# Optimization experiments

Measured on AMD Instinct MI355X. Metric: run time of the kernel, lower is better.

Reference implementation:

```python
import jax, jax.numpy as jnp
import numpy as np

D = 4096   # feature_dim
L = 24     # num_vision_layers
H = 8      # num_heads
HD = D // H
R = D // 4 # reduced_dim


def _ln(x, g, b, eps=1e-5):
    m = jnp.mean(x, -1, keepdims=True)
    v = jnp.var(x, -1, keepdims=True)
    return (x - m) * jax.lax.rsqrt(v + eps) * g + b


def setup_inputs() -> dict:
    key = jax.random.key(0)
    ks = jax.random.split(key, 16)
    B, T, N = 1, 128, 576
    def W(k, shape, s=0.02):
        return jax.random.normal(k, shape, jnp.float32) * s
    inp = {
        'text': jax.random.normal(ks[0], (B, T, D), jnp.float32),
        'feats': jax.random.normal(ks[1], (L, B, N, D), jnp.float32),
        'W1_w': W(ks[2], (R, 3 * D)), 'W1_b': jnp.zeros((R,), jnp.float32),
        'Wc_w': W(ks[3], (D, R)), 'Wc_b': jnp.zeros((D,), jnp.float32),
        'Wi_w': W(ks[4], (D, R)), 'Wi_b': jnp.zeros((D,), jnp.float32),
        'Wf_w': W(ks[5], (D, R)), 'Wf_b': jnp.zeros((D,), jnp.float32),
        'bc': jnp.zeros((D,), jnp.float32),
        'bi': jnp.zeros((D,), jnp.float32),
        'bf': jnp.zeros((D,), jnp.float32),
        'g1_w': W(ks[6], (D, D)), 'g1_b': jnp.zeros((D,), jnp.float32),
        'g2_w': W(ks[7], (D, D)), 'g2_b': jnp.zeros((D,), jnp.float32),
        'Wq_w': W(ks[8], (D, D)), 'Wq_b': jnp.zeros((D,), jnp.float32),
        'Wk_w': W(ks[9], (D, D)), 'Wk_b': jnp.zeros((D,), jnp.float32),
        'Wo_w': W(ks[10], (D, D)), 'Wo_b': jnp.zeros((D,), jnp.float32),
        'qn_g': jnp.ones((D,), jnp.float32), 'qn_b': jnp.zeros((D,), jnp.float32),
        'kn_g': jnp.ones((D,), jnp.float32), 'kn_b': jnp.zeros((D,), jnp.float32),
        'on_g': jnp.ones((D,), jnp.float32), 'on_b': jnp.zeros((D,), jnp.float32),
    }
    return inp


def reference(text, feats, W1_w, W1_b, Wc_w, Wc_b, Wi_w, Wi_b, Wf_w, Wf_b,
              bc, bi, bf, g1_w, g1_b, g2_w, g2_b, Wq_w, Wq_b, Wk_w, Wk_b,
              Wo_w, Wo_b, qn_g, qn_b, kn_g, kn_b, on_g, on_b):
    B, T, _ = text.shape
    N = feats.shape[2]
    text_global = jnp.mean(text, axis=1)      # [B, D]
    y = jnp.mean(feats, axis=2)               # [L, B, D]

    # DSU recurrence over L layers (shared weights) via scan
    def step(c_prev, y_l):
        cpn = jax.nn.sigmoid(jax.lax.stop_gradient(c_prev))
        comb = jnp.concatenate([cpn, y_l, text_global], axis=-1)  # [B, 3D]
        s = jax.nn.relu(comb @ W1_w.T + W1_b)                     # [B, R]
        c_tilde = jnp.tanh(s @ Wc_w.T + Wc_b + bc)
        ig = jax.nn.sigmoid(s @ Wi_w.T + Wi_b + bi)
        fg = jax.nn.sigmoid(s @ Wf_w.T + Wf_b + bf)
        c = fg * c_prev + ig * c_tilde
        return c, c

    _, ctx = jax.lax.scan(step, jnp.zeros_like(text_global), y)   # [L, B, D]

    # Spatial gate, vectorized over all L layers (context is detached)
    c_sg = jax.lax.stop_gradient(ctx)[:, :, None, :]              # [L, B, 1, D]
    h = jax.nn.gelu((c_sg + feats) @ g1_w.T + g1_b, approximate=False)
    gate = jax.nn.sigmoid(h @ g2_w.T + g2_b)
    refreshed = feats * gate                                      # [L, B, N, D]

    # Q / K / V
    Q = _ln(text @ Wq_w.T + Wq_b, qn_g, qn_b)
    Q = Q.reshape(B, T, H, HD).transpose(0, 2, 1, 3)              # [B, H, T, HD]
    K = _ln(refreshed @ Wk_w.T + Wk_b, kn_g, kn_b)                # [L, B, N, D]
    K_all = K.reshape(L, B, N, H, HD).transpose(1, 3, 0, 2, 4).reshape(B, H, L * N, HD)
    V_all = refreshed.reshape(L, B, N, H, HD).transpose(1, 3, 0, 2, 4).reshape(B, H, L * N, HD)

    scale = (HD ** 0.5) * (L ** 0.5)
    scores = jnp.einsum('bhtd,bhsd->bhts', Q, K_all) / scale
    attn = jax.nn.softmax(scores, axis=-1)
    att = jnp.einsum('bhts,bhsd->bhtd', attn, V_all)
    att = att.transpose(0, 2, 1, 3).reshape(B, T, D)
    out = _ln(att @ Wo_w.T + Wo_b, on_g, on_b)
    return out
```

## Files before the change

kernel.cpp:

```cpp
#include <hip/hip_runtime.h>

#define USH unsigned short

__device__ __forceinline__ float bf2f(USH u) {
    return __uint_as_float(((unsigned int)u) << 16);
}
__device__ __forceinline__ float bfbits2f(unsigned int b) {
    return __uint_as_float(b << 16);
}
__device__ __forceinline__ USH f2bf(float f) {
    unsigned int x = __float_as_uint(f);
    x += 0x7fffu + ((x >> 16) & 1u);
    return (USH)(x >> 16);
}
__device__ __forceinline__ unsigned int pack2bf(float a, float b) {
    return (unsigned int)f2bf(a) | ((unsigned int)f2bf(b) << 16);
}
__device__ __forceinline__ float sigmoidf_(float x) { return 1.0f / (1.0f + expf(-x)); }

typedef __bf16 bf16x8 __attribute__((ext_vector_type(8)));
typedef float floatx4 __attribute__((ext_vector_type(4)));

#define GLOAD_LDS16(g, l) __builtin_amdgcn_global_load_lds( \
    (const __attribute__((address_space(1))) void*)(g),     \
    (__attribute__((address_space(3))) void*)(l), 16, 0, 0)

enum { EPI_SCORES = 0, EPI_GELU = 1, EPI_GATE = 2, EPI_PLAIN = 3 };

template <int EPI, bool WF32>
__global__ __launch_bounds__(256)
void gemm_bt(const USH* __restrict__ A, int lda, long long sAz, long long sAz2, int zdiv,
             const void* __restrict__ Wv, int ldw, long long sWz, long long sWz2,
             void* __restrict__ Cout, int ldc, long long sCz,
             const float* __restrict__ bias, const float* __restrict__ fmul,
             float alpha, int Kd)
{
    __shared__ USH As[2][128 * 32];
    __shared__ USH Ws[2][128 * 32];
    const int z = blockIdx.z;
    const int z1 = z / zdiv;
    const int z2 = z % zdiv;
    A += (size_t)z1 * (size_t)sAz + (size_t)z2 * (size_t)sAz2;
    const USH* Wb = (const USH*)Wv + (size_t)z1 * (size_t)sWz + (size_t)z2 * (size_t)sWz2;
    const float* Wf = (const float*)Wv;
    const int m0 = blockIdx.y * 128;
    const int n0 = blockIdx.x * 128;
    const int tid = threadIdx.x;
    const int lane = tid & 63;
    const int wid = tid >> 6;
    const int wm = (wid >> 1) * 64;
    const int wn = (wid & 1) * 64;
    const int q = lane >> 4;
    const int r = lane & 15;

    floatx4 acc[4][4] = {};

    const int c0 = wid * 2;
    const int grow = c0 * 16 + (lane >> 2);
    const int gcol = (lane & 3) * 8;
    const USH* apA0 = A + (size_t)(m0 + grow) * lda + gcol;
    const USH* apA1 = apA0 + (size_t)16 * lda;
    USH* lA0 = &As[0][c0 * 512];
    USH* lA1 = &As[0][(c0 + 1) * 512];
    const USH* apW0 = Wb + (size_t)(n0 + grow) * ldw + gcol;
    const USH* apW1 = apW0 + (size_t)16 * ldw;
    USH* lW0 = &Ws[0][c0 * 512];
    USH* lW1 = &Ws[0][(c0 + 1) * 512];

    const int frow = tid >> 1;
    const int fcol = (tid & 1) * 16;
    const float* wpf = Wf + (size_t)(n0 + frow) * ldw + fcol;
    USH* wsw = &Ws[0][frow * 32 + fcol];

    auto stage = [&](int k0, int b) {
        GLOAD_LDS16(apA0 + k0, lA0 + b * 4096);
        GLOAD_LDS16(apA1 + k0, lA1 + b * 4096);
        if constexpr (WF32) {
            float4 f0 = *reinterpret_cast<const float4*>(wpf + k0);
            float4 f1 = *reinterpret_cast<const float4*>(wpf + k0 + 4);
            float4 f2 = *reinterpret_cast<const float4*>(wpf + k0 + 8);
            float4 f3 = *reinterpret_cast<const float4*>(wpf + k0 + 12);
            uint4 w0, w1;
            w0.x = pack2bf(f0.x, f0.y); w0.y = pack2bf(f0.z, f0.w);
            w0.z = pack2bf(f1.x, f1.y); w0.w = pack2bf(f1.z, f1.w);
            w1.x = pack2bf(f2.x, f2.y); w1.y = pack2bf(f2.z, f2.w);
            w1.z = pack2bf(f3.x, f3.y); w1.w = pack2bf(f3.z, f3.w);
            *reinterpret_cast<uint4*>(wsw + b * 4096) = w0;
            *reinterpret_cast<uint4*>(wsw + b * 4096 + 8) = w1;
        } else {
            GLOAD_LDS16(apW0 + k0, lW0 + b * 4096);
            GLOAD_LDS16(apW1 + k0, lW1 + b * 4096);
        }
    };

    auto compute = [&](const USH* Asb, const USH* Wsb) {
        bf16x8 af[4], wf4[4];
#pragma unroll
        for (int i = 0; i < 4; i++)
            af[i] = *reinterpret_cast<const bf16x8*>(&Asb[(wm + i * 16 + r) * 32 + q * 8]);
#pragma unroll
        for (int j = 0; j < 4; j++)
            wf4[j] = *reinterpret_cast<const bf16x8*>(&Wsb[(wn + j * 16 + r) * 32 + q * 8]);
#pragma unroll
        for (int i = 0; i < 4; i++)
#pragma unroll
            for (int j = 0; j < 4; j++)
                acc[i][j] = __builtin_amdgcn_mfma_f32_16x16x32_bf16(af[i], wf4[j], acc[i][j], 0, 0, 0);
    };

    stage(0, 0);
    asm volatile("s_waitcnt vmcnt(0) lgkmcnt(0)" ::: "memory");
    __builtin_amdgcn_s_barrier();

    for (int k0 = 0; k0 < Kd; k0 += 64) {
        stage(k0 + 32, 1);
        compute(&As[0][0], &Ws[0][0]);
        asm volatile("s_waitcnt vmcnt(0) lgkmcnt(0)" ::: "memory");
        __builtin_amdgcn_s_barrier();
        if (k0 + 64 < Kd) stage(k0 + 64, 0);
        compute(&As[1][0], &Ws[1][0]);
        if (k0 + 64 < Kd) {
            asm volatile("s_waitcnt vmcnt(0) lgkmcnt(0)" ::: "memory");
            __builtin_amdgcn_s_barrier();
        }
    }

#pragma unroll
    for (int j = 0; j < 4; j++) {
        const int col = n0 + wn + j * 16 + r;
        const float bv = (EPI == EPI_SCORES) ? 0.f : bias[col];
#pragma unroll
        for (int i = 0; i < 4; i++) {
            const int row0 = m0 + wm + i * 16 + q * 4;
#pragma unroll
            for (int rr = 0; rr < 4; rr++) {
                const int row = row0 + rr;
                float v = acc[i][j][rr];
                if (EPI == EPI_SCORES) {
                    ((float*)Cout)[(size_t)z * (size_t)sCz + (size_t)row * ldc + col] = v * alpha;
                } else if (EPI == EPI_GELU) {
                    v += bv;
                    float g = 0.5f * v * (1.0f + erff(v * 0.7071067811865475f));
                    ((USH*)Cout)[(size_t)row * ldc + col] = f2bf(g);
                } else if (EPI == EPI_GATE) {
                    v += bv;
                    float gate = 1.0f / (1.0f + expf(-v));
                    float o = gate * fmul[(size_t)row * ldc + col];
                    ((USH*)Cout)[(size_t)row * ldc + col] = f2bf(o);
                } else {
                    ((USH*)Cout)[(size_t)row * ldc + col] = f2bf(v + bv);
                }
            }
        }
    }
}

__global__ __launch_bounds__(256)
void means_k(const float* __restrict__ text, const float* __restrict__ feats,
             float* __restrict__ tg, float* __restrict__ yv, float* __restrict__ cst,
             float* __restrict__ scs)
{
    const int d = blockIdx.x * 256 + threadIdx.x;
    const int z = blockIdx.y;
    if (z < 24) {
        const float* f = feats + (size_t)z * 576 * 4096 + d;
        float s = 0.f;
        for (int n = 0; n < 576; n++) s += f[(size_t)n * 4096];
        yv[z * 4096 + d] = s * (1.0f / 576.0f);
    } else if (z == 24) {
        float s = 0.f;
        for (int t = 0; t < 128; t++) s += text[(size_t)t * 4096 + d];
        tg[d] = s * (1.0f / 128.0f);
    } else {
        cst[d] = 0.f;
        scs[d] = 0.5f;
    }
}

__global__ __launch_bounds__(256)
void f32_to_bf16(const float* __restrict__ src, USH* __restrict__ dst)
{
    const size_t base = ((size_t)blockIdx.x * 256 + threadIdx.x) * 8;
    float4 f0 = *reinterpret_cast<const float4*>(src + base);
    float4 f1 = *reinterpret_cast<const float4*>(src + base + 4);
    uint4 ov;
    ov.x = pack2bf(f0.x, f0.y); ov.y = pack2bf(f0.z, f0.w);
    ov.z = pack2bf(f1.x, f1.y); ov.w = pack2bf(f1.z, f1.w);
    *reinterpret_cast<uint4*>(dst + base) = ov;
}

__global__ __launch_bounds__(256)
void transpose_bf16(const USH* __restrict__ src, USH* __restrict__ dst)
{
    __shared__ USH T[64][72];
    const int s0 = blockIdx.x * 64;
    const int d0 = blockIdx.y * 64;
    const int tid = threadIdx.x;
    const int rr = tid >> 3;
    const int c8 = (tid & 7) * 8;
#pragma unroll
    for (int i = 0; i < 2; i++) {
        const int row = rr + i * 32;
        uint4 v = *reinterpret_cast<const uint4*>(src + (size_t)(s0 + row) * 4096 + d0 + c8);
        *reinterpret_cast<uint4*>(&T[row][c8]) = v;
    }
    __syncthreads();
#pragma unroll
    for (int i = 0; i < 2; i++) {
        const int drow = rr + i * 32;
        USH tmp[8];
#pragma unroll
        for (int j = 0; j < 8; j++) tmp[j] = T[c8 + j][drow];
        *reinterpret_cast<uint4*>(dst + (size_t)(d0 + drow) * 13824 + s0 + c8) =
            *reinterpret_cast<const uint4*>(tmp);
    }
}

__global__ __launch_bounds__(256)
void pv_reduce(const float* __restrict__ part, USH* __restrict__ att)
{
    const int idx = blockIdx.x * 256 + threadIdx.x;
    const size_t o = (size_t)idx * 4;
    const int t = (int)(o >> 12);
    const int col = (int)(o & 4095);
    const int h = col >> 9;
    const int d = col & 511;
    const float* p = part + (size_t)h * 8 * 65536 + t * 512 + d;
    float4 s = {0.f, 0.f, 0.f, 0.f};
#pragma unroll
    for (int kc = 0; kc < 8; kc++) {
        float4 v = *reinterpret_cast<const float4*>(p + (size_t)kc * 65536);
        s.x += v.x; s.y += v.y; s.z += v.z; s.w += v.w;
    }
    uint2 ov;
    ov.x = pack2bf(s.x, s.y);
    ov.y = pack2bf(s.z, s.w);
    *reinterpret_cast<uint2*>(att + o) = ov;
}

__global__ __launch_bounds__(256)
void dsu_pre(const float* __restrict__ W1w, const float* __restrict__ W1b,
             const float* __restrict__ yv, const float* __restrict__ tg,
             float* __restrict__ pre)
{
    const int rrow = blockIdx.x;
    const float* w = W1w + (size_t)rrow * 12288;
    const int tid = threadIdx.x;
    float wy[16];
    float at = 0.f;
#pragma unroll
    for (int i = 0; i < 16; i++) {
        const int k = tid + i * 256;
        wy[i] = w[4096 + k];
        at += w[8192 + k] * tg[k];
    }
#pragma unroll
    for (int o = 32; o > 0; o >>= 1) at += __shfl_down(at, o, 64);
    __shared__ float red[4];
    __shared__ float tgs;
    if ((tid & 63) == 0) red[tid >> 6] = at;
    __syncthreads();
    if (tid == 0) tgs = red[0] + red[1] + red[2] + red[3] + W1b[rrow];
    for (int l = 0; l < 24; l++) {
        const float* y = yv + (size_t)l * 4096;
        float a = 0.f;
#pragma unroll
        for (int i = 0; i < 16; i++) a += wy[i] * y[tid + i * 256];
#pragma unroll
        for (int o = 32; o > 0; o >>= 1) a += __shfl_down(a, o, 64);
        __syncthreads();
        if ((tid & 63) == 0) red[tid >> 6] = a;
        __syncthreads();
        if (tid == 0) pre[l * 1024 + rrow] = red[0] + red[1] + red[2] + red[3] + tgs;
    }
}

__global__ __launch_bounds__(256)
void dsu_s1(const float* __restrict__ W1w, const float* __restrict__ scs,
            const float* __restrict__ pre_l, float* __restrict__ sv)
{
    const int rrow = blockIdx.x;
    const float* w = W1w + (size_t)rrow * 12288;
    const int tid = threadIdx.x;
    float acc = 0.f;
#pragma unroll
    for (int i = 0; i < 16; i++) {
        const int k = tid + i * 256;
        acc += w[k] * scs[k];
    }
#pragma unroll
    for (int o = 32; o > 0; o >>= 1) acc += __shfl_down(acc, o, 64);
    __shared__ float red[4];
    if ((tid & 63) == 0) red[tid >> 6] = acc;
    __syncthreads();
    if (tid == 0) {
        float t = red[0] + red[1] + red[2] + red[3] + pre_l[rrow];
        sv[rrow] = fmaxf(t, 0.f);
    }
}

__global__ __launch_bounds__(256)
void dsu_s2(const float* __restrict__ Wc, const float* __restrict__ Wcb,
            const float* __restrict__ Wi, const float* __restrict__ Wib,
            const float* __restrict__ Wf, const float* __restrict__ Wfb,
            const float* __restrict__ bc, const float* __restrict__ bi,
            const float* __restrict__ bfv,
             const float* __restrict__ sv, float* __restrict__ c,
             float* __restrict__ ctx_l, float* __restrict__ scs)
{
    const int d = blockIdx.x;
    const int tid = threadIdx.x;
    float a0 = 0.f, a1 = 0.f, a2 = 0.f;
    for (int k = tid; k < 1024; k += 256) {
        float s = sv[k];
        a0 += Wc[(size_t)d * 1024 + k] * s;
        a1 += Wi[(size_t)d * 1024 + k] * s;
        a2 += Wf[(size_t)d * 1024 + k] * s;
    }
#pragma unroll
    for (int o = 32; o > 0; o >>= 1) {
        a0 += __shfl_down(a0, o, 64);
        a1 += __shfl_down(a1, o, 64);
        a2 += __shfl_down(a2, o, 64);
    }
    __shared__ float red[3][4];
    if ((tid & 63) == 0) {
        red[0][tid >> 6] = a0; red[1][tid >> 6] = a1; red[2][tid >> 6] = a2;
    }
    __syncthreads();
    if (tid == 0) {
        float A0 = red[0][0] + red[0][1] + red[0][2] + red[0][3];
        float A1 = red[1][0] + red[1][1] + red[1][2] + red[1][3];
        float A2 = red[2][0] + red[2][1] + red[2][2] + red[2][3];
        float ct = tanhf(A0 + Wcb[d] + bc[d]);
        float ig = sigmoidf_(A1 + Wib[d] + bi[d]);
        float fg = sigmoidf_(A2 + Wfb[d] + bfv[d]);
        float cn = fg * c[d] + ig * ct;
        c[d] = cn;
        ctx_l[d] = cn;
        scs[d] = sigmoidf_(cn);
    }
}

__global__ __launch_bounds__(256)
void make_x(const float* __restrict__ feats, const float* __restrict__ ctx,
            USH* __restrict__ X)
{
    const size_t base = ((size_t)blockIdx.x * 256 + threadIdx.x) * 8;
    const int row = (int)(base >> 12);
    const int l = row / 576;
    const float* cr = ctx + (size_t)l * 4096 + (base & 4095);
    float4 f0 = *reinterpret_cast<const float4*>(feats + base);
    float4 f1 = *reinterpret_cast<const float4*>(feats + base + 4);
    uint4 ov;
    ov.x = pack2bf(f0.x + cr[0], f0.y + cr[1]);
    ov.y = pack2bf(f0.z + cr[2], f0.w + cr[3]);
    ov.z = pack2bf(f1.x + cr[4], f1.y + cr[5]);
    ov.w = pack2bf(f1.z + cr[6], f1.w + cr[7]);
    *reinterpret_cast<uint4*>(X + base) = ov;
}

template <bool OUTF32>
__global__ __launch_bounds__(256)
void ln_rows(const USH* __restrict__ in, void* __restrict__ out,
             const float* __restrict__ g, const float* __restrict__ b)
{
    const int row = blockIdx.x;
    const USH* x = in + (size_t)row * 4096;
    const int tid = threadIdx.x;
    float vals[16];
    float s = 0.f, ss = 0.f;
#pragma unroll
    for (int i = 0; i < 16; i++) {
        float v = bf2f(x[tid + i * 256]);
        vals[i] = v; s += v; ss += v * v;
    }
#pragma unroll
    for (int off = 32; off > 0; off >>= 1) {
        s += __shfl_down(s, off, 64);
        ss += __shfl_down(ss, off, 64);
    }
    __shared__ float rs[4], rss[4];
    __shared__ float stats[2];
    if ((tid & 63) == 0) { rs[tid >> 6] = s; rss[tid >> 6] = ss; }
    __syncthreads();
    if (tid == 0) {
        float S = rs[0] + rs[1] + rs[2] + rs[3];
        float SS = rss[0] + rss[1] + rss[2] + rss[3];
        float mean = S * (1.0f / 4096.0f);
        float var = SS * (1.0f / 4096.0f) - mean * mean;
        stats[0] = mean;
        stats[1] = rsqrtf(var + 1e-5f);
    }
    __syncthreads();
    const float mean = stats[0], rstd = stats[1];
#pragma unroll
    for (int i = 0; i < 16; i++) {
        const int cidx = tid + i * 256;
        float v = (vals[i] - mean) * rstd * g[cidx] + b[cidx];
        if (OUTF32) ((float*)out)[(size_t)row * 4096 + cidx] = v;
        else ((USH*)out)[(size_t)row * 4096 + cidx] = f2bf(v);
    }
}

__global__ __launch_bounds__(256)
void softmax_rows(const float* __restrict__ scores, USH* __restrict__ probs)
{
    const int row = blockIdx.x;
    const float* x = scores + (size_t)row * 13824;
    USH* p = probs + (size_t)row * 13824;
    const int tid = threadIdx.x;
    float mx = -1e30f;
    for (int i = tid; i < 13824; i += 256) mx = fmaxf(mx, x[i]);
#pragma unroll
    for (int off = 32; off > 0; off >>= 1) mx = fmaxf(mx, __shfl_down(mx, off, 64));
    __shared__ float rm[4];
    __shared__ float bm, bs;
    if ((tid & 63) == 0) rm[tid >> 6] = mx;
    __syncthreads();
    if (tid == 0) bm = fmaxf(fmaxf(rm[0], rm[1]), fmaxf(rm[2], rm[3]));
    __syncthreads();
    const float M = bm;
    float sum = 0.f;
    for (int i = tid; i < 13824; i += 256) sum += expf(x[i] - M);
#pragma unroll
    for (int off = 32; off > 0; off >>= 1) sum += __shfl_down(sum, off, 64);
    if ((tid & 63) == 0) rm[tid >> 6] = sum;
    __syncthreads();
    if (tid == 0) bs = 1.0f / (rm[0] + rm[1] + rm[2] + rm[3]);
    __syncthreads();
    const float inv = bs;
    for (int i = tid; i < 13824; i += 256) p[i] = f2bf(expf(x[i] - M) * inv);
}

extern "C" void kernel_launch(void* const* d_in, const int* in_sizes, int n_in,
                              void* d_out, int out_size, void* d_ws, size_t ws_size,
                              hipStream_t stream)
{
    const float* text = (const float*)d_in[0];
    const float* feats = (const float*)d_in[1];
    const float* W1w = (const float*)d_in[2];
    const float* W1b = (const float*)d_in[3];
    const float* Wcw = (const float*)d_in[4];
    const float* Wcb = (const float*)d_in[5];
    const float* Wiw = (const float*)d_in[6];
    const float* Wib = (const float*)d_in[7];
    const float* Wfw = (const float*)d_in[8];
    const float* Wfb = (const float*)d_in[9];
    const float* bc  = (const float*)d_in[10];
    const float* bi  = (const float*)d_in[11];
    const float* bfv = (const float*)d_in[12];
    const float* g1w = (const float*)d_in[13];
    const float* g1b = (const float*)d_in[14];
    const float* g2w = (const float*)d_in[15];
    const float* g2b = (const float*)d_in[16];
    const float* Wqw = (const float*)d_in[17];
    const float* Wqb = (const float*)d_in[18];
    const float* Wkw = (const float*)d_in[19];
    const float* Wkb = (const float*)d_in[20];
    const float* Wow = (const float*)d_in[21];
    const float* Wob = (const float*)d_in[22];
    const float* qng = (const float*)d_in[23];
    const float* qnb = (const float*)d_in[24];
    const float* kng = (const float*)d_in[25];
    const float* knb = (const float*)d_in[26];
    const float* ong = (const float*)d_in[27];
    const float* onb = (const float*)d_in[28];

    char* base = (char*)d_ws;
    size_t off = 0;
    auto take = [&](size_t nbytes) -> char* {
        char* p = base + off;
        off += (nbytes + 255) & ~(size_t)255;
        return p;
    };
    const size_t BIG = (size_t)13824 * 4096 * 2;
    USH* P1 = (USH*)take(BIG);
    USH* P2 = (USH*)take(BIG);
    USH* P3 = (USH*)take(BIG);
    float* tg  = (float*)take(4096 * 4);
    float* yv  = (float*)take(24 * 4096 * 4);
    float* cst = (float*)take(4096 * 4);
    float* scs = (float*)take(4096 * 4);
    float* sv  = (float*)take(1024 * 4);
    float* pre = (float*)take(24 * 1024 * 4);
    float* ctx = (float*)take(24 * 4096 * 4);
    USH* textb = (USH*)take((size_t)128 * 4096 * 2);
    USH* Qb   = (USH*)take((size_t)128 * 4096 * 2);
    USH* attb = (USH*)take((size_t)128 * 4096 * 2);
    USH* opre = (USH*)take((size_t)128 * 4096 * 2);
    USH* wb   = (USH*)take((size_t)4096 * 4096 * 2);
    float* scores = (float*)P2;
    USH* probs = (USH*)((char*)P2 + (size_t)8 * 128 * 13824 * 4);
    USH* vT = P1;
    float* pvpart = (float*)wb;
    (void)ws_size; (void)in_sizes; (void)n_in; (void)out_size;

    means_k<<<dim3(16, 26), 256, 0, stream>>>(text, feats, tg, yv, cst, scs);
    f32_to_bf16<<<256, 256, 0, stream>>>(text, textb);
    dsu_pre<<<1024, 256, 0, stream>>>(W1w, W1b, yv, tg, pre);

    for (int l = 0; l < 24; l++) {
        dsu_s1<<<1024, 256, 0, stream>>>(W1w, scs, pre + (size_t)l * 1024, sv);
        dsu_s2<<<4096, 256, 0, stream>>>(Wcw, Wcb, Wiw, Wib, Wfw, Wfb, bc, bi, bfv,
                                         sv, cst, ctx + (size_t)l * 4096, scs);
    }

    make_x<<<27648, 256, 0, stream>>>(feats, ctx, P1);
    f32_to_bf16<<<8192, 256, 0, stream>>>(g1w, wb);
    gemm_bt<EPI_GELU, false><<<dim3(32, 108, 1), 256, 0, stream>>>(
        P1, 4096, 0, 0, 1, wb, 4096, 0, 0, P2, 4096, 0, g1b, nullptr, 1.f, 4096);
    f32_to_bf16<<<8192, 256, 0, stream>>>(g2w, wb);
    gemm_bt<EPI_GATE, false><<<dim3(32, 108, 1), 256, 0, stream>>>(
        P2, 4096, 0, 0, 1, wb, 4096, 0, 0, P3, 4096, 0, g2b, feats, 1.f, 4096);

    f32_to_bf16<<<8192, 256, 0, stream>>>(Wkw, wb);
    gemm_bt<EPI_PLAIN, false><<<dim3(32, 108, 1), 256, 0, stream>>>(
        P3, 4096, 0, 0, 1, wb, 4096, 0, 0, P1, 4096, 0, Wkb, nullptr, 1.f, 4096);
    ln_rows<false><<<13824, 256, 0, stream>>>(P1, P1, kng, knb);

    gemm_bt<EPI_PLAIN, true><<<dim3(32, 1, 1), 256, 0, stream>>>(
        textb, 4096, 0, 0, 1, Wqw, 4096, 0, 0, Qb, 4096, 0, Wqb, nullptr, 1.f, 4096);
    ln_rows<false><<<128, 256, 0, stream>>>(Qb, Qb, qng, qnb);

    const float alpha = 0.00902109753f;
    gemm_bt<EPI_SCORES, false><<<dim3(108, 1, 8), 256, 0, stream>>>(
        Qb, 4096, 512, 0, 1, P1, 4096, 512, 0, scores, 13824, (long long)128 * 13824,
        nullptr, nullptr, alpha, 512);

    transpose_bf16<<<dim3(216, 64), 256, 0, stream>>>(P3, vT);
    softmax_rows<<<1024, 256, 0, stream>>>(scores, probs);
    gemm_bt<EPI_SCORES, false><<<dim3(4, 1, 64), 256, 0, stream>>>(
        probs, 13824, (long long)128 * 13824, 1728, 8,
        vT, 13824, (long long)512 * 13824, 1728,
        pvpart, 512, 65536,
        nullptr, nullptr, 1.0f, 1728);
    pv_reduce<<<512, 256, 0, stream>>>(pvpart, attb);

    gemm_bt<EPI_PLAIN, true><<<dim3(32, 1, 1), 256, 0, stream>>>(
        attb, 4096, 0, 0, 1, Wow, 4096, 0, 0, opre, 4096, 0, Wob, nullptr, 1.f, 4096);
    ln_rows<true><<<128, 256, 0, stream>>>(opre, (float*)d_out, ong, onb);
}
```

Baseline: 3.950 ms.

## Add 256x256-tile 512-thread bf16 GEMM for the three big projections

Introduces a new GEMM kernel with 256x256 output tiles, 8 waves, K-step 64, swizzled LDS, double-buffered direct global-to-LDS loads interleaved with MFMA phases, s_setprio around the MFMA bursts, and an XCD-aware block-to-tile mapping. It replaces the 128x128 gemm_bt for the gate1, gate2 and K projections (13824x4096x4096 each), which dominate runtime. The aim is higher arithmetic intensity per LDS byte and better L2 locality per XCD. The cost is much larger register and LDS use per block (about 128KB of LDS), which may limit occupancy, and a layout that assumes dimensions of exactly 4096.

```diff
diff --git a/kernel.cpp b/kernel.cpp
--- a/kernel.cpp
+++ b/kernel.cpp
@@ -26,6 +26,145 @@
     (__attribute__((address_space(3))) void*)(l), 16, 0, 0)
 
 enum { EPI_SCORES = 0, EPI_GELU = 1, EPI_GATE = 2, EPI_PLAIN = 3 };
+
+template <int QA, int QB>
+__device__ __forceinline__ void phase256(const USH* __restrict__ Ab,
+                                         const USH* __restrict__ Bb,
+                                         floatx4 (&acc)[8][4],
+                                         int q, int r, int wn)
+{
+    bf16x8 af[4][2], wf[2][2];
+#pragma unroll
+    for (int ii = 0; ii < 4; ii++) {
+        const int row = (QA * 4 + ii) * 16 + r;
+#pragma unroll
+        for (int ks = 0; ks < 2; ks++)
+            af[ii][ks] = *reinterpret_cast<const bf16x8*>(
+                Ab + row * 64 + (((q + ks * 4) ^ (r & 7)) * 8));
+    }
+#pragma unroll
+    for (int jj = 0; jj < 2; jj++) {
+        const int row = (wn & 1) * 64 + (QB * 2 + jj) * 16 + r;
+#pragma unroll
+        for (int ks = 0; ks < 2; ks++)
+            wf[jj][ks] = *reinterpret_cast<const bf16x8*>(
+                Bb + row * 64 + (((q + ks * 4) ^ (r & 7)) * 8));
+    }
+    __builtin_amdgcn_s_setprio(1);
+#pragma unroll
+    for (int ii = 0; ii < 4; ii++)
+#pragma unroll
+        for (int jj = 0; jj < 2; jj++) {
+            acc[QA * 4 + ii][QB * 2 + jj] = __builtin_amdgcn_mfma_f32_16x16x32_bf16(
+                af[ii][0], wf[jj][0], acc[QA * 4 + ii][QB * 2 + jj], 0, 0, 0);
+            acc[QA * 4 + ii][QB * 2 + jj] = __builtin_amdgcn_mfma_f32_16x16x32_bf16(
+                af[ii][1], wf[jj][1], acc[QA * 4 + ii][QB * 2 + jj], 0, 0, 0);
+        }
+    __builtin_amdgcn_s_setprio(0);
+}
+
+template <int EPI>
+__global__ __launch_bounds__(512, 2)
+void gemm256(const USH* __restrict__ A, const USH* __restrict__ W,
+             void* __restrict__ Cout, const float* __restrict__ bias,
+             const float* __restrict__ fmul, int Kd)
+{
+    __shared__ __align__(16) USH As[32768];
+    __shared__ __align__(16) USH Ws[32768];
+
+    const int bid = blockIdx.x;
+    const int xcd = bid & 7;
+    const int j = bid >> 3;
+    const int bn = xcd * 2 + (j & 1);
+    const int bm = j >> 1;
+    const int m0 = bm * 256, n0 = bn * 256;
+
+    const int tid = threadIdx.x;
+    const int lane = tid & 63;
+    const int wid = tid >> 6;
+    const int wm = wid >> 2;
+    const int wn = wid & 3;
+    const int bh = wn >> 1;
+    const int q = lane >> 4, r = lane & 15;
+
+    floatx4 acc[8][4] = {};
+
+    const int sl = lane >> 3;
+    const int sc = ((lane & 7) ^ sl) * 8;
+    const USH* gA[2][2]; const USH* gW[2][2];
+    USH* lA[2][2]; USH* lW[2][2];
+#pragma unroll
+    for (int h = 0; h < 2; h++)
+#pragma unroll
+        for (int i = 0; i < 2; i++) {
+            const int seg = wid * 2 + i;
+            gA[h][i] = A + (size_t)(m0 + h * 128 + seg * 8 + sl) * 4096 + sc;
+            gW[h][i] = W + (size_t)(n0 + h * 128 + seg * 8 + sl) * 4096 + sc;
+            lA[h][i] = As + h * 8192 + seg * 512;
+            lW[h][i] = Ws + h * 8192 + seg * 512;
+        }
+
+#pragma unroll
+    for (int h = 0; h < 2; h++)
+#pragma unroll
+        for (int i = 0; i < 2; i++) {
+            GLOAD_LDS16(gA[h][i], lA[h][i]);
+            GLOAD_LDS16(gW[h][i], lW[h][i]);
+        }
+    __syncthreads();
+
+    const int nt = Kd >> 6;
+    for (int t = 0; t < nt; t++) {
+        const int p = t & 1;
+        const USH* Ab = As + wm * 8192 + p * 16384;
+        const USH* Bb = Ws + bh * 8192 + p * 16384;
+        const int ko = (t + 1) * 64;
+        const int bo = (p ^ 1) * 16384;
+        const bool st = (t + 1 < nt);
+        if (st) {
+            GLOAD_LDS16(gA[0][0] + ko, lA[0][0] + bo);
+            GLOAD_LDS16(gA[0][1] + ko, lA[0][1] + bo);
+            GLOAD_LDS16(gA[1][0] + ko, lA[1][0] + bo);
+            GLOAD_LDS16(gA[1][1] + ko, lA[1][1] + bo);
+        }
+        phase256<0, 0>(Ab, Bb, acc, q, r, wn);
+        if (st) {
+            GLOAD_LDS16(gW[0][0] + ko, lW[0][0] + bo);
+            GLOAD_LDS16(gW[0][1] + ko, lW[0][1] + bo);
+            GLOAD_LDS16(gW[1][0] + ko, lW[1][0] + bo);
+            GLOAD_LDS16(gW[1][1] + ko, lW[1][1] + bo);
+        }
+        phase256<0, 1>(Ab, Bb, acc, q, r, wn);
+        phase256<1, 0>(Ab, Bb, acc, q, r, wn);
+        phase256<1, 1>(Ab, Bb, acc, q, r, wn);
+        __syncthreads();
+    }
+
+#pragma unroll
+    for (int jt = 0; jt < 4; jt++) {
+        const int col = n0 + wn * 64 + jt * 16 + r;
+        const float bv = bias[col];
+#pragma unroll
+        for (int i = 0; i < 8; i++) {
+            const int row0 = m0 + wm * 128 + i * 16 + q * 4;
+#pragma unroll
+            for (int rr = 0; rr < 4; rr++) {
+                const int row = row0 + rr;
+                float v = acc[i][jt][rr] + bv;
+                if (EPI == EPI_GELU) {
+                    float g = 0.5f * v * (1.0f + erff(v * 0.7071067811865475f));
+                    ((USH*)Cout)[(size_t)row * 4096 + col] = f2bf(g);
+                } else if (EPI == EPI_GATE) {
+                    float gate = 1.0f / (1.0f + expf(-v));
+                    float o = gate * fmul[(size_t)row * 4096 + col];
+                    ((USH*)Cout)[(size_t)row * 4096 + col] = f2bf(o);
+                } else {
+                    ((USH*)Cout)[(size_t)row * 4096 + col] = f2bf(v);
+                }
+            }
+        }
+    }
+}
 
 template <int EPI, bool WF32>
 __global__ __launch_bounds__(256)
@@ -508,15 +647,12 @@
 
     make_x<<<27648, 256, 0, stream>>>(feats, ctx, P1);
     f32_to_bf16<<<8192, 256, 0, stream>>>(g1w, wb);
-    gemm_bt<EPI_GELU, false><<<dim3(32, 108, 1), 256, 0, stream>>>(
-        P1, 4096, 0, 0, 1, wb, 4096, 0, 0, P2, 4096, 0, g1b, nullptr, 1.f, 4096);
+    gemm256<EPI_GELU><<<864, 512, 0, stream>>>(P1, wb, P2, g1b, nullptr, 4096);
     f32_to_bf16<<<8192, 256, 0, stream>>>(g2w, wb);
-    gemm_bt<EPI_GATE, false><<<dim3(32, 108, 1), 256, 0, stream>>>(
-        P2, 4096, 0, 0, 1, wb, 4096, 0, 0, P3, 4096, 0, g2b, feats, 1.f, 4096);
+    gemm256<EPI_GATE><<<864, 512, 0, stream>>>(P2, wb, P3, g2b, feats, 4096);
 
     f32_to_bf16<<<8192, 256, 0, stream>>>(Wkw, wb);
-    gemm_bt<EPI_PLAIN, false><<<dim3(32, 108, 1), 256, 0, stream>>>(
-        P3, 4096, 0, 0, 1, wb, 4096, 0, 0, P1, 4096, 0, Wkb, nullptr, 1.f, 4096);
+    gemm256<EPI_PLAIN><<<864, 512, 0, stream>>>(P3, wb, P1, Wkb, nullptr, 4096);
     ln_rows<false><<<13824, 256, 0, stream>>>(P1, P1, kng, knb);
 
     gemm_bt<EPI_PLAIN, true><<<dim3(32, 1, 1), 256, 0, stream>>>(
```

Measured after the change: 3.657 ms. 7.4% less time.
